# Performance work log

Hardware: AMD Instinct MI355X
Metric: run time of the kernel (lower is better)

## Reference

```python
import jax, jax.numpy as jnp
import numpy as np

B, C, H, W = 256, 1024, 7, 7
D_HID, N_CLS = 768, 5

def setup_inputs() -> dict:
    key = jax.random.key(0)
    k1, k2, k3, k4, k5 = jax.random.split(key, 5)
    flat = C * H * W  # 50176
    return {
        "features": jax.random.normal(k1, (B, C, H, W), dtype=jnp.float32),
        "W1": jax.random.normal(k2, (D_HID, flat), dtype=jnp.float32) * 0.02,
        "b1": jax.random.normal(k3, (D_HID,), dtype=jnp.float32) * 0.02,
        "W2": jax.random.normal(k4, (N_CLS, D_HID), dtype=jnp.float32) * 0.02,
        "b2": jax.random.normal(k5, (N_CLS,), dtype=jnp.float32) * 0.02,
    }

def reference(features, W1, b1, W2, b2):
    # PCAM: per-(batch, channel) global max over spatial dims, broadcast-multiplied
    # back onto the feature map. Replaces the torch Python double loop with one
    # fused reduce-max + elementwise multiply.
    ch_max = jnp.max(features, axis=(2, 3), keepdims=True)  # [B, C, 1, 1]
    pcams = features * ch_max                               # [B, C, H, W]
    flat = pcams.reshape(pcams.shape[0], -1)                # [B, C*H*W]
    h = jax.nn.relu(flat @ W1.T + b1)                       # [B, 768]
    logits = h @ W2.T + b2                                  # [B, num_classes]
    return (logits, features)
```

## Files before the change

### kernel.cpp

```cpp
#include <hip/hip_runtime.h>
#include <hip/hip_bf16.h>

#define B_SZ   256
#define C_SZ   1024
#define HW     49
#define KDIM   50176
#define DHID   768
#define NCLS   5

typedef __bf16 bf16x8 __attribute__((ext_vector_type(8)));
typedef __bf16 bf16x4 __attribute__((ext_vector_type(4)));
typedef float  f32x4  __attribute__((ext_vector_type(4)));

#define GLOAD_LDS16(gsrc, ldst) \
  __builtin_amdgcn_global_load_lds((__attribute__((address_space(1))) void*)(gsrc), \
                                   (__attribute__((address_space(3))) void*)(ldst), 16, 0, 0)

__global__ __launch_bounds__(256) void pcam_kernel(const float* __restrict__ feat,
                                                   float* __restrict__ feat_out,
                                                   __bf16* __restrict__ pcam) {
  __shared__ float sv[1568];
  __shared__ float smax[32];
  const int tid = threadIdx.x;
  const size_t base = (size_t)blockIdx.x * 1568;

  const float4* src4 = (const float4*)(feat + base);
  float4* dst4 = (float4*)(feat_out + base);
  #pragma unroll
  for (int i = 0; i < 2; ++i) {
    int idx = tid + i * 256;
    if (idx < 392) {
      float4 v = src4[idx];
      dst4[idx] = v;
      ((float4*)sv)[idx] = v;
    }
  }
  __syncthreads();

  {
    const int r = tid >> 3, p = tid & 7;
    float mx = -INFINITY;
    for (int i = p; i < HW; i += 8) mx = fmaxf(mx, sv[r * HW + i]);
    #pragma unroll
    for (int off = 1; off < 8; off <<= 1) mx = fmaxf(mx, __shfl_xor(mx, off));
    if (p == 0) smax[r] = mx;
  }
  __syncthreads();

  for (int i = tid; i < 1568; i += 256) {
    int r = (i * 1338) >> 16;
    float v = sv[i] * smax[r];
    pcam[base + i] = (__bf16)v;
  }
}

#define BM 128
#define BN 128
#define BK 64
#define MT 2
#define NT 6
#define KSPLIT 42
#define KSTEPS 784

__global__ __launch_bounds__(512, 4) void gemm1_kernel(const __bf16* __restrict__ pcam,
                                                       const float* __restrict__ W1,
                                                       float* __restrict__ h_acc) {
  __shared__ __bf16 Asm[2][BM * BK];
  __shared__ __bf16 Bsm[2][BN * BK];

  const int tid  = threadIdx.x;
  const int lane = tid & 63;
  const int w    = tid >> 6;
  const int wm   = w >> 2;
  const int wn   = w & 3;
  const int bx   = blockIdx.x;
  const int m0   = (bx & 1) * BM;
  const int n0   = (bx >> 1) * BN;
  const int ks   = blockIdx.y;
  const int s0   = (ks * KSTEPS) / KSPLIT;
  const int s1   = ((ks + 1) * KSTEPS) / KSPLIT;

  const int nb = tid >> 4;
  const int kq = tid & 15;
  const int kb = kq >> 1;
  const int sub = (kq & 1) << 3;

  f32x4 acc[4][2];
  #pragma unroll
  for (int i = 0; i < 4; ++i)
    #pragma unroll
    for (int j = 0; j < 2; ++j) acc[i][j] = f32x4{0.f, 0.f, 0.f, 0.f};

  float4 br0, br1, br2, br3;

#define LOAD_B(s) do { \
    const size_t koff_ = (size_t)(s) * BK + kq * 4; \
    br0 = *(const float4*)(W1 + (size_t)(n0 + 0  + nb) * KDIM + koff_); \
    br1 = *(const float4*)(W1 + (size_t)(n0 + 32 + nb) * KDIM + koff_); \
    br2 = *(const float4*)(W1 + (size_t)(n0 + 64 + nb) * KDIM + koff_); \
    br3 = *(const float4*)(W1 + (size_t)(n0 + 96 + nb) * KDIM + koff_); \
  } while (0)

#define STAGE_A(bi, s) do { \
    const int k0_ = (s) * BK; \
    _Pragma("unroll") \
    for (int it = 0; it < 2; ++it) { \
      const int q   = it * 512 + tid; \
      const int m   = q >> 3; \
      const int kbl = (q & 7) ^ (m & 7); \
      const __bf16* src = pcam + (size_t)(m0 + m) * KDIM + k0_ + kbl * 8; \
      GLOAD_LDS16(src, &Asm[bi][(size_t)(it * 512 + w * 64) * 8]); \
    } \
  } while (0)

#define WRITE_B(bi) do { \
    _Pragma("unroll") \
    for (int it = 0; it < 4; ++it) { \
      const float4 v = (it == 0) ? br0 : (it == 1) ? br1 : (it == 2) ? br2 : br3; \
      bf16x4 bv; \
      bv[0] = (__bf16)v.x; bv[1] = (__bf16)v.y; bv[2] = (__bf16)v.z; bv[3] = (__bf16)v.w; \
      const int n = it * 32 + nb; \
      const int phys = n * 128 + (((kb ^ (n & 7)) << 4) | sub); \
      *(bf16x4*)((char*)Bsm[bi] + phys) = bv; \
    } \
  } while (0)

#define COMPUTE(bi) do { \
    _Pragma("unroll") \
    for (int ksub = 0; ksub < 2; ++ksub) { \
      bf16x8 af[4], bfr[2]; \
      const int kb2 = ksub * 4 + (lane >> 4); \
      _Pragma("unroll") \
      for (int i = 0; i < 4; ++i) { \
        const int m = wm * 64 + i * 16 + (lane & 15); \
        af[i] = *(const bf16x8*)((const char*)Asm[bi] + m * 128 + ((kb2 ^ (m & 7)) << 4)); \
      } \
      _Pragma("unroll") \
      for (int j = 0; j < 2; ++j) { \
        const int n = wn * 32 + j * 16 + (lane & 15); \
        bfr[j] = *(const bf16x8*)((const char*)Bsm[bi] + n * 128 + ((kb2 ^ (n & 7)) << 4)); \
      } \
      _Pragma("unroll") \
      for (int i = 0; i < 4; ++i) \
        _Pragma("unroll") \
        for (int j = 0; j < 2; ++j) \
          acc[i][j] = __builtin_amdgcn_mfma_f32_16x16x32_bf16(af[i], bfr[j], acc[i][j], 0, 0, 0); \
    } \
  } while (0)

  LOAD_B(s0);
  STAGE_A(0, s0);
  WRITE_B(0);
  __syncthreads();

  int buf = 0;
  for (int s = s0; s < s1; ++s) {
    const int nxt = s + 1;
    if (nxt < s1) {
      LOAD_B(nxt);
      STAGE_A(buf ^ 1, nxt);
    }
    COMPUTE(buf);
    if (nxt < s1) WRITE_B(buf ^ 1);
    __syncthreads();
    buf ^= 1;
  }

  #pragma unroll
  for (int i = 0; i < 4; ++i) {
    const int mb = m0 + wm * 64 + i * 16 + (lane >> 4) * 4;
    #pragma unroll
    for (int j = 0; j < 2; ++j) {
      const int n = n0 + wn * 32 + j * 16 + (lane & 15);
      #pragma unroll
      for (int r = 0; r < 4; ++r)
        unsafeAtomicAdd(&h_acc[(size_t)(mb + r) * DHID + n], acc[i][j][r]);
    }
  }
#undef LOAD_B
#undef STAGE_A
#undef WRITE_B
#undef COMPUTE
}

__global__ __launch_bounds__(64) void head_kernel(const float* __restrict__ h_acc,
                                                  const float* __restrict__ b1,
                                                  const float* __restrict__ W2,
                                                  const float* __restrict__ b2,
                                                  float* __restrict__ logits) {
  const int m = blockIdx.x;
  const int lane = threadIdx.x;
  float hv[12];
  #pragma unroll
  for (int j = 0; j < 12; ++j) {
    float v = h_acc[(size_t)m * DHID + j * 64 + lane] + b1[j * 64 + lane];
    hv[j] = v > 0.f ? v : 0.f;
  }
  #pragma unroll
  for (int c = 0; c < NCLS; ++c) {
    float s = 0.f;
    #pragma unroll
    for (int j = 0; j < 12; ++j) s += hv[j] * W2[c * DHID + j * 64 + lane];
    #pragma unroll
    for (int off = 32; off > 0; off >>= 1) s += __shfl_xor(s, off);
    if (lane == 0) logits[m * NCLS + c] = s + b2[c];
  }
}

extern "C" void kernel_launch(void* const* d_in, const int* in_sizes, int n_in,
                              void* d_out, int out_size, void* d_ws, size_t ws_size,
                              hipStream_t stream) {
  const float* feat = (const float*)d_in[0];
  const float* W1   = (const float*)d_in[1];
  const float* b1   = (const float*)d_in[2];
  const float* W2   = (const float*)d_in[3];
  const float* b2   = (const float*)d_in[4];

  float* logits   = (float*)d_out;
  float* feat_out = (float*)d_out + (size_t)B_SZ * NCLS;

  __bf16* pcam  = (__bf16*)d_ws;
  float*  h_acc = (float*)((char*)d_ws + (size_t)B_SZ * KDIM * 2);

  hipMemsetAsync(h_acc, 0, (size_t)B_SZ * DHID * sizeof(float), stream);
  pcam_kernel<<<(B_SZ * C_SZ) / 32, 256, 0, stream>>>(feat, feat_out, pcam);
  gemm1_kernel<<<dim3(MT * NT, KSPLIT), 512, 0, stream>>>(pcam, W1, h_acc);
  head_kernel<<<B_SZ, 64, 0, stream>>>(h_acc, b1, W2, b2, logits);
}
```

Before: 112.4 us.

## Deepen GEMM prefetch to two stages and replace atomic split-K with partial-sum reduce

The GEMM now prefetches W1 two K-steps ahead using two register sets. A tiles are loaded through registers and written to LDS by hand instead of using global_load_lds. Split-K results are written as per-split partials and summed in a new reduce kernel that also applies bias and ReLU, which removes the float atomics and the memset. The cost is higher register pressure, a partial buffer of about 33 MB that must be written and read back, and one extra kernel launch.

```diff
diff --git a/kernel.cpp b/kernel.cpp
--- a/kernel.cpp
+++ b/kernel.cpp
@@ -11,10 +11,6 @@
 typedef __bf16 bf16x8 __attribute__((ext_vector_type(8)));
 typedef __bf16 bf16x4 __attribute__((ext_vector_type(4)));
 typedef float  f32x4  __attribute__((ext_vector_type(4)));
-
-#define GLOAD_LDS16(gsrc, ldst) \
-  __builtin_amdgcn_global_load_lds((__attribute__((address_space(1))) void*)(gsrc), \
-                                   (__attribute__((address_space(3))) void*)(ldst), 16, 0, 0)
 
 __global__ __launch_bounds__(256) void pcam_kernel(const float* __restrict__ feat,
                                                    float* __restrict__ feat_out,
@@ -64,7 +60,7 @@
 
 __global__ __launch_bounds__(512, 4) void gemm1_kernel(const __bf16* __restrict__ pcam,
                                                        const float* __restrict__ W1,
-                                                       float* __restrict__ h_acc) {
+                                                       float* __restrict__ h_part) {
   __shared__ __bf16 Asm[2][BM * BK];
   __shared__ __bf16 Bsm[2][BN * BK];
 
@@ -80,10 +76,15 @@
   const int s0   = (ks * KSTEPS) / KSPLIT;
   const int s1   = ((ks + 1) * KSTEPS) / KSPLIT;
 
-  const int nb = tid >> 4;
-  const int kq = tid & 15;
-  const int kb = kq >> 1;
+  const int nb  = tid >> 4;
+  const int kq  = tid & 15;
+  const int kb  = kq >> 1;
   const int sub = (kq & 1) << 3;
+  const int ma  = tid >> 2;
+  const int kb0 = (tid & 3) * 2;
+
+  const float* wbase = W1 + (size_t)(n0 + nb) * KDIM + kq * 4;
+  const __bf16* abase = pcam + (size_t)(m0 + ma) * KDIM + kb0 * 8;
 
   f32x4 acc[4][2];
   #pragma unroll
@@ -91,38 +92,41 @@
     #pragma unroll
     for (int j = 0; j < 2; ++j) acc[i][j] = f32x4{0.f, 0.f, 0.f, 0.f};
 
-  float4 br0, br1, br2, br3;
-
-#define LOAD_B(s) do { \
-    const size_t koff_ = (size_t)(s) * BK + kq * 4; \
-    br0 = *(const float4*)(W1 + (size_t)(n0 + 0  + nb) * KDIM + koff_); \
-    br1 = *(const float4*)(W1 + (size_t)(n0 + 32 + nb) * KDIM + koff_); \
-    br2 = *(const float4*)(W1 + (size_t)(n0 + 64 + nb) * KDIM + koff_); \
-    br3 = *(const float4*)(W1 + (size_t)(n0 + 96 + nb) * KDIM + koff_); \
-  } while (0)
-
-#define STAGE_A(bi, s) do { \
-    const int k0_ = (s) * BK; \
-    _Pragma("unroll") \
-    for (int it = 0; it < 2; ++it) { \
-      const int q   = it * 512 + tid; \
-      const int m   = q >> 3; \
-      const int kbl = (q & 7) ^ (m & 7); \
-      const __bf16* src = pcam + (size_t)(m0 + m) * KDIM + k0_ + kbl * 8; \
-      GLOAD_LDS16(src, &Asm[bi][(size_t)(it * 512 + w * 64) * 8]); \
-    } \
-  } while (0)
-
-#define WRITE_B(bi) do { \
+  float4 bA0, bA1, bA2, bA3;
+  float4 bB0, bB1, bB2, bB3;
+  bf16x8 ar0, ar1;
+
+#define LOAD_B(R0, R1, R2, R3, s) do { \
+    const size_t ko_ = (size_t)(s) * BK; \
+    R0 = *(const float4*)(wbase + ko_); \
+    R1 = *(const float4*)(wbase + (size_t)32 * KDIM + ko_); \
+    R2 = *(const float4*)(wbase + (size_t)64 * KDIM + ko_); \
+    R3 = *(const float4*)(wbase + (size_t)96 * KDIM + ko_); \
+  } while (0)
+
+#define LOAD_A(s) do { \
+    const __bf16* p_ = abase + (size_t)(s) * BK; \
+    ar0 = *(const bf16x8*)(p_); \
+    ar1 = *(const bf16x8*)(p_ + 8); \
+  } while (0)
+
+#define WRITE_B(bi, R0, R1, R2, R3) do { \
     _Pragma("unroll") \
     for (int it = 0; it < 4; ++it) { \
-      const float4 v = (it == 0) ? br0 : (it == 1) ? br1 : (it == 2) ? br2 : br3; \
+      const float4 v = (it == 0) ? R0 : (it == 1) ? R1 : (it == 2) ? R2 : R3; \
       bf16x4 bv; \
       bv[0] = (__bf16)v.x; bv[1] = (__bf16)v.y; bv[2] = (__bf16)v.z; bv[3] = (__bf16)v.w; \
       const int n = it * 32 + nb; \
       const int phys = n * 128 + (((kb ^ (n & 7)) << 4) | sub); \
       *(bf16x4*)((char*)Bsm[bi] + phys) = bv; \
     } \
+  } while (0)
+
+#define WRITE_A(bi) do { \
+    const int p0 = ma * 128 + (((kb0 ^ (ma & 7)) << 4)); \
+    const int p1 = ma * 128 + ((((kb0 + 1) ^ (ma & 7)) << 4)); \
+    *(bf16x8*)((char*)Asm[bi] + p0) = ar0; \
+    *(bf16x8*)((char*)Asm[bi] + p1) = ar1; \
   } while (0)
 
 #define COMPUTE(bi) do { \
@@ -148,43 +152,62 @@
     } \
   } while (0)
 
-  LOAD_B(s0);
-  STAGE_A(0, s0);
-  WRITE_B(0);
+  LOAD_B(bA0, bA1, bA2, bA3, s0);
+  if (s0 + 1 < s1) LOAD_B(bB0, bB1, bB2, bB3, s0 + 1);
+  LOAD_A(s0);
+  WRITE_B(s0 & 1, bA0, bA1, bA2, bA3);
+  WRITE_A(s0 & 1);
+  if (s0 + 1 < s1) LOAD_A(s0 + 1);
   __syncthreads();
 
-  int buf = 0;
   for (int s = s0; s < s1; ++s) {
-    const int nxt = s + 1;
-    if (nxt < s1) {
-      LOAD_B(nxt);
-      STAGE_A(buf ^ 1, nxt);
-    }
-    COMPUTE(buf);
-    if (nxt < s1) WRITE_B(buf ^ 1);
+    const int cur = s & 1;
+    const int rel = (s ^ s0) & 1;
+    if (s + 2 < s1) {
+      if (rel) LOAD_B(bB0, bB1, bB2, bB3, s + 2);
+      else     LOAD_B(bA0, bA1, bA2, bA3, s + 2);
+    }
+    if (s + 1 < s1) {
+      if (rel) WRITE_B(cur ^ 1, bA0, bA1, bA2, bA3);
+      else     WRITE_B(cur ^ 1, bB0, bB1, bB2, bB3);
+    }
+    COMPUTE(cur);
+    if (s + 1 < s1) WRITE_A(cur ^ 1);
+    if (s + 2 < s1) LOAD_A(s + 2);
     __syncthreads();
-    buf ^= 1;
-  }
-
+  }
+
+  float* out = h_part + (size_t)ks * DHID * B_SZ;
   #pragma unroll
   for (int i = 0; i < 4; ++i) {
     const int mb = m0 + wm * 64 + i * 16 + (lane >> 4) * 4;
     #pragma unroll
     for (int j = 0; j < 2; ++j) {
       const int n = n0 + wn * 32 + j * 16 + (lane & 15);
-      #pragma unroll
-      for (int r = 0; r < 4; ++r)
-        unsafeAtomicAdd(&h_acc[(size_t)(mb + r) * DHID + n], acc[i][j][r]);
+      *(f32x4*)(out + (size_t)n * B_SZ + mb) = acc[i][j];
     }
   }
 #undef LOAD_B
-#undef STAGE_A
+#undef LOAD_A
 #undef WRITE_B
+#undef WRITE_A
 #undef COMPUTE
 }
 
-__global__ __launch_bounds__(64) void head_kernel(const float* __restrict__ h_acc,
-                                                  const float* __restrict__ b1,
+__global__ __launch_bounds__(256) void reduce_kernel(const float* __restrict__ h_part,
+                                                     const float* __restrict__ b1,
+                                                     float* __restrict__ h) {
+  const int n = blockIdx.x;
+  const int m = threadIdx.x;
+  float s = 0.f;
+  #pragma unroll 6
+  for (int ks = 0; ks < KSPLIT; ++ks)
+    s += h_part[((size_t)ks * DHID + n) * B_SZ + m];
+  float v = s + b1[n];
+  h[(size_t)m * DHID + n] = v > 0.f ? v : 0.f;
+}
+
+__global__ __launch_bounds__(64) void head_kernel(const float* __restrict__ h,
                                                   const float* __restrict__ W2,
                                                   const float* __restrict__ b2,
                                                   float* __restrict__ logits) {
@@ -192,10 +215,7 @@
   const int lane = threadIdx.x;
   float hv[12];
   #pragma unroll
-  for (int j = 0; j < 12; ++j) {
-    float v = h_acc[(size_t)m * DHID + j * 64 + lane] + b1[j * 64 + lane];
-    hv[j] = v > 0.f ? v : 0.f;
-  }
+  for (int j = 0; j < 12; ++j) hv[j] = h[(size_t)m * DHID + j * 64 + lane];
   #pragma unroll
   for (int c = 0; c < NCLS; ++c) {
     float s = 0.f;
@@ -219,11 +239,14 @@
   float* logits   = (float*)d_out;
   float* feat_out = (float*)d_out + (size_t)B_SZ * NCLS;
 
-  __bf16* pcam  = (__bf16*)d_ws;
-  float*  h_acc = (float*)((char*)d_ws + (size_t)B_SZ * KDIM * 2);
-
-  hipMemsetAsync(h_acc, 0, (size_t)B_SZ * DHID * sizeof(float), stream);
+  char* ws = (char*)d_ws;
+  __bf16* pcam   = (__bf16*)ws;
+  float*  h_part = (float*)(ws + (size_t)B_SZ * KDIM * 2);
+  float*  h      = (float*)(ws + (size_t)B_SZ * KDIM * 2
+                               + (size_t)KSPLIT * DHID * B_SZ * 4);
+
   pcam_kernel<<<(B_SZ * C_SZ) / 32, 256, 0, stream>>>(feat, feat_out, pcam);
-  gemm1_kernel<<<dim3(MT * NT, KSPLIT), 512, 0, stream>>>(pcam, W1, h_acc);
-  head_kernel<<<B_SZ, 64, 0, stream>>>(h_acc, b1, W2, b2, logits);
-}
+  gemm1_kernel<<<dim3(MT * NT, KSPLIT), 512, 0, stream>>>(pcam, W1, h_part);
+  reduce_kernel<<<DHID, 256, 0, stream>>>(h_part, b1, h);
+  head_kernel<<<B_SZ, 64, 0, stream>>>(h, W2, b2, logits);
+}
```

Result: faster. 107.9 us (-4.0%).
